# Kernel tuning notes

Measured on AMD Instinct MI355X. Metric: run time of the kernel, lower is better.

## Reference

```python
import jax, jax.numpy as jnp
import numpy as np
import math

HIDDEN = 1024
EXPAND = 2
INNER = HIDDEN * EXPAND          # 2048
STATE = 16
K = 4                            # conv kernel size
DT_RANK = math.ceil(HIDDEN / 16) # 64
DT_MIN, DT_MAX = 1e-3, 0.1


def setup_inputs() -> dict:
    key = jax.random.key(0)
    ks = jax.random.split(key, 10)
    B, L = 2, 1024
    hidden_states = jax.random.normal(ks[0], (B, L, HIDDEN), dtype=jnp.float32)
    # parameters (torch Linear weight stored transposed -> we use [in, out])
    W_in = jax.random.normal(ks[1], (HIDDEN, 2 * INNER), dtype=jnp.float32) * (HIDDEN ** -0.5)
    conv_w = jax.random.normal(ks[2], (K, INNER), dtype=jnp.float32) * (K ** -0.5)   # depthwise
    conv_b = jax.random.normal(ks[3], (INNER,), dtype=jnp.float32) * 0.02
    W_xproj = jax.random.normal(ks[4], (INNER, DT_RANK + 2 * STATE), dtype=jnp.float32) * (INNER ** -0.5)
    dt_init_std = DT_RANK ** -0.5
    W_dt = jax.random.uniform(ks[5], (DT_RANK, INNER), dtype=jnp.float32,
                              minval=-dt_init_std, maxval=dt_init_std)
    dt = jnp.exp(jax.random.uniform(ks[6], (INNER,), dtype=jnp.float32)
                 * (math.log(DT_MAX) - math.log(DT_MIN)) + math.log(DT_MIN))
    dt = jnp.clip(dt, 1e-4, None)
    b_dt = dt + jnp.log(-jnp.expm1(-dt))   # inverse softplus init
    A = jnp.tile(jnp.arange(1, STATE + 1, dtype=jnp.float32)[None, :], (INNER, 1))
    A_log = jnp.log(A)
    D = jnp.ones((INNER,), dtype=jnp.float32)
    W_out = jax.random.normal(ks[7], (INNER, HIDDEN), dtype=jnp.float32) * (INNER ** -0.5)
    return {"hidden_states": hidden_states, "W_in": W_in, "conv_w": conv_w,
            "conv_b": conv_b, "W_xproj": W_xproj, "W_dt": W_dt, "b_dt": b_dt,
            "A_log": A_log, "D": D, "W_out": W_out}


def _silu(x):
    return x * jax.nn.sigmoid(x)


def _mamba_forward(hidden_states, W_in, conv_w, conv_b, W_xproj, W_dt, b_dt, A_log, D, W_out):
    Bsz, L, _ = hidden_states.shape
    xz = hidden_states @ W_in                # [B, L, 2*inner]
    x, z = jnp.split(xz, 2, axis=-1)         # each [B, L, inner]

    # causal depthwise conv along L (torch Conv1d pad=K-1, truncated to seq_len)
    xp = jnp.pad(x, ((0, 0), (K - 1, 0), (0, 0)))
    xc = conv_b
    for k in range(K):                       # K=4 fixed, unrolled
        xc = xc + xp[:, k:k + L, :] * conv_w[k]
    x = _silu(xc)                            # [B, L, inner]

    # selective SSM
    A = -jnp.exp(A_log)                      # [inner, state]
    xproj = x @ W_xproj                      # [B, L, dt_rank + 2*state]
    dt, Bm, Cm = jnp.split(xproj, [DT_RANK, DT_RANK + STATE], axis=-1)
    dt = jax.nn.softplus(dt @ W_dt + b_dt)   # [B, L, inner]

    deltaA = jnp.exp(dt[..., None] * A)                                   # [B, L, inner, state]
    deltaBx = dt[..., None] * Bm[:, :, None, :] * x[..., None]            # [B, L, inner, state]

    def step(h, inp):
        dA, dBx, c = inp                     # [B,inner,state],[B,inner,state],[B,state]
        h = dA * h + dBx
        y = jnp.einsum('bdn,bn->bd', h, c)   # [B, inner]
        return h, y

    h0 = jnp.zeros((Bsz, INNER, STATE), dtype=x.dtype)
    _, ys = jax.lax.scan(step, h0, (jnp.moveaxis(deltaA, 1, 0),
                                    jnp.moveaxis(deltaBx, 1, 0),
                                    jnp.moveaxis(Cm, 1, 0)))
    y = jnp.moveaxis(ys, 0, 1)               # [B, L, inner]
    y = y + x * D
    y = y * _silu(z)
    return y @ W_out                         # [B, L, hidden]


def reference(hidden_states, W_in, conv_w, conv_b, W_xproj, W_dt, b_dt, A_log, D, W_out):
    return _mamba_forward(hidden_states, W_in, conv_w, conv_b, W_xproj, W_dt, b_dt, A_log, D, W_out)
```

## Files before the change

### kernel.cpp

```cpp
#include <hip/hip_runtime.h>
#include <math.h>

#define HID    1024
#define INNER  2048
#define NROWS  2048
#define LSEQ   1024
#define STATE  16
#define DTR    64
#define XPN    96
#define NC     32
#define LC     32
#define KSPLIT 16
#define KCH    128

typedef __attribute__((ext_vector_type(8))) short bf16x8;
typedef __attribute__((ext_vector_type(4))) float f32x4;

#define GLDS16(g, l) __builtin_amdgcn_global_load_lds( \
    (const __attribute__((address_space(1))) unsigned int*)(g), \
    (__attribute__((address_space(3))) unsigned int*)(l), 16, 0, 0)

__device__ __forceinline__ float siluf(float x) { return x / (1.f + __expf(-x)); }

__device__ __forceinline__ short f2bf(float f) {
    unsigned u = __float_as_uint(f);
    unsigned r = (u + 0x7FFFu + ((u >> 16) & 1u)) >> 16;
    return (short)r;
}
__device__ __forceinline__ float bf2f(short s) {
    return __uint_as_float(((unsigned)(unsigned short)s) << 16);
}

template<int N> __device__ __forceinline__ void wait_vm() {
    if      constexpr (N == 0) asm volatile("s_waitcnt vmcnt(0)" ::: "memory");
    else if constexpr (N == 2) asm volatile("s_waitcnt vmcnt(2)" ::: "memory");
    else if constexpr (N == 3) asm volatile("s_waitcnt vmcnt(3)" ::: "memory");
    else if constexpr (N == 4) asm volatile("s_waitcnt vmcnt(4)" ::: "memory");
}

__global__ __launch_bounds__(256) void prep1(
    const float* __restrict__ hs, short* __restrict__ hs16,
    const float* __restrict__ W_in, short* __restrict__ W_inT,
    const float* __restrict__ W_xp, short* __restrict__ W_xpT,
    const float* __restrict__ W_dt, short* __restrict__ W_dtT,
    const float* __restrict__ W_out, short* __restrict__ W_outT)
{
    int blk = blockIdx.x;
    if (blk < 2048) {
        int i = blk * 256 + threadIdx.x;
        float4 v = ((const float4*)hs)[i];
        union { short s[4]; int2 p; } o;
        o.s[0] = f2bf(v.x); o.s[1] = f2bf(v.y); o.s[2] = f2bf(v.z); o.s[3] = f2bf(v.w);
        ((int2*)hs16)[i] = o.p;
        return;
    }
    blk -= 2048;
    const float* W; short* Wt; int K, N, bx, by;
    if (blk < 4096)        { W = W_in;  Wt = W_inT;  K = 1024; N = 4096; bx = blk & 127; by = blk >> 7; }
    else if (blk < 4288)   { int t = blk - 4096; W = W_xp;  Wt = W_xpT;  K = 2048; N = 96;   bx = t % 3;  by = t / 3; }
    else if (blk < 4416)   { int t = blk - 4288; W = W_dt;  Wt = W_dtT;  K = 64;   N = 2048; bx = t & 63; by = t >> 6; }
    else                   { int t = blk - 4416; W = W_out; Wt = W_outT; K = 2048; N = 1024; bx = t & 31; by = t >> 5; }
    __shared__ float tile[32][33];
    int bn = bx * 32, bk = by * 32;
    int tx = threadIdx.x & 31, ty = threadIdx.x >> 5;
#pragma unroll
    for (int i = 0; i < 32; i += 8)
        tile[ty + i][tx] = W[(size_t)(bk + ty + i) * N + bn + tx];
    __syncthreads();
#pragma unroll
    for (int i = 0; i < 32; i += 8)
        Wt[(size_t)(bn + ty + i) * K + bk + tx] = f2bf(tile[tx][ty + i]);
}

template<int BM, int BN, int EPI>
__global__ __launch_bounds__(256) void gemm_p(
    const short* __restrict__ A, const short* __restrict__ Bt,
    void* __restrict__ Cout, int M, int N, int K,
    const float* __restrict__ bias)
{
    constexpr int NI = BM / 32;
    constexpr int NJ = BN / 32;
    constexpr int LPB = BM / 64 + BN / 64;
    __shared__ short As[3][BM * 32];
    __shared__ short Bs[3][BN * 32];
    const int tid = threadIdx.x;
    const int lane = tid & 63;
    const int wv = tid >> 6;
    const int wm = (wv >> 1) * (BM / 2), wn = (wv & 1) * (BN / 2);
    const int bm = blockIdx.y * BM, bn = blockIdx.x * BN;
    const int l16 = lane & 15, lhi = lane >> 4;
    const size_t arow0 = (size_t)(bm + wv * 16 + (lane >> 2)) * K + (lane & 3) * 8;
    const size_t brow0 = (size_t)(bn + wv * 16 + (lane >> 2)) * K + (lane & 3) * 8;

    auto stage = [&](int buf, int koff) {
        GLDS16(&A[arow0 + koff], &As[buf][(wv * 16) * 32]);
        if (BM == 128) GLDS16(&A[arow0 + (size_t)64 * K + koff], &As[buf][(64 + wv * 16) * 32]);
        GLDS16(&Bt[brow0 + koff], &Bs[buf][(wv * 16) * 32]);
        if (BN == 128) GLDS16(&Bt[brow0 + (size_t)64 * K + koff], &Bs[buf][(64 + wv * 16) * 32]);
    };

    f32x4 acc[NI][NJ] = {};
    const int nt = K / 32;
    stage(0, 0);
    if (nt > 1) stage(1, 32);
    for (int t = 0; t < nt; ++t) {
        if (t == nt - 1) wait_vm<0>();
        else             wait_vm<LPB>();
        __builtin_amdgcn_s_barrier();
        __builtin_amdgcn_sched_barrier(0);
        if (t + 2 < nt) stage((t + 2) % 3, (t + 2) * 32);
        const int cur = t % 3;
        bf16x8 af[NI], bfr[NJ];
#pragma unroll
        for (int i = 0; i < NI; ++i)
            af[i] = *(const bf16x8*)&As[cur][(wm + i * 16 + l16) * 32 + lhi * 8];
#pragma unroll
        for (int j = 0; j < NJ; ++j)
            bfr[j] = *(const bf16x8*)&Bs[cur][(wn + j * 16 + l16) * 32 + lhi * 8];
#pragma unroll
        for (int i = 0; i < NI; ++i)
#pragma unroll
            for (int j = 0; j < NJ; ++j)
                acc[i][j] = __builtin_amdgcn_mfma_f32_16x16x32_bf16(af[i], bfr[j], acc[i][j], 0, 0, 0);
    }
#pragma unroll
    for (int i = 0; i < NI; ++i)
#pragma unroll
        for (int j = 0; j < NJ; ++j)
#pragma unroll
            for (int r = 0; r < 4; ++r) {
                int row = bm + wm + i * 16 + lhi * 4 + r;
                int col = bn + wn + j * 16 + l16;
                float v = acc[i][j][r];
                if (EPI == 0) {
                    ((float*)Cout)[(size_t)row * N + col] = v;
                } else if (EPI == 1) {
                    v += bias[col];
                    v = (v > 20.f) ? v : log1pf(__expf(v));
                    ((short*)Cout)[(size_t)row * N + col] = f2bf(v);
                } else {
                    ((short*)Cout)[(size_t)row * N + col] = f2bf(v);
                }
            }
}

__global__ __launch_bounds__(256) void gemm_xproj(
    const short* __restrict__ A, const short* __restrict__ Bt,
    float* __restrict__ partial)
{
    __shared__ short As[4][64][40];
    __shared__ short Bs[4][96][40];
    const int tid = threadIdx.x;
    const int lane = tid & 63;
    const int wv = tid >> 6;
    const int l16 = lane & 15, lhi = lane >> 4;
    const int bm = blockIdx.x * 64;
    const int kc = blockIdx.y;
    const int k0 = kc * KCH;
    const int r = tid >> 2, cs = (tid & 3) * 8;
#pragma unroll
    for (int ks = 0; ks < 4; ++ks)
        *(int4*)&As[ks][r][cs] = *(const int4*)&A[(size_t)(bm + r) * INNER + k0 + ks * 32 + cs];
#pragma unroll
    for (int ks = 0; ks < 4; ++ks)
        *(int4*)&Bs[ks][r][cs] = *(const int4*)&Bt[(size_t)r * INNER + k0 + ks * 32 + cs];
    if (tid < 128) {
        int r2 = 64 + (tid >> 2);
#pragma unroll
        for (int ks = 0; ks < 4; ++ks)
            *(int4*)&Bs[ks][r2][cs] = *(const int4*)&Bt[(size_t)r2 * INNER + k0 + ks * 32 + cs];
    }
    __syncthreads();
    f32x4 acc[6] = {};
#pragma unroll
    for (int ks = 0; ks < 4; ++ks) {
        bf16x8 a = *(const bf16x8*)&As[ks][wv * 16 + l16][lhi * 8];
#pragma unroll
        for (int j = 0; j < 6; ++j) {
            bf16x8 b = *(const bf16x8*)&Bs[ks][j * 16 + l16][lhi * 8];
            acc[j] = __builtin_amdgcn_mfma_f32_16x16x32_bf16(a, b, acc[j], 0, 0, 0);
        }
    }
    size_t base = (size_t)kc * ((size_t)NROWS * XPN);
#pragma unroll
    for (int j = 0; j < 6; ++j)
#pragma unroll
        for (int rr = 0; rr < 4; ++rr) {
            int row = bm + wv * 16 + lhi * 4 + rr;
            int col = j * 16 + l16;
            partial[base + (size_t)row * XPN + col] = acc[j][rr];
        }
}

__global__ __launch_bounds__(256) void xproj_reduce(
    const float* __restrict__ partial, float* __restrict__ xproj,
    short* __restrict__ xprojb)
{
    int idx = blockIdx.x * 256 + threadIdx.x;
    if (idx >= NROWS * XPN) return;
    float s = 0.f;
#pragma unroll
    for (int kc = 0; kc < KSPLIT; ++kc)
        s += partial[(size_t)kc * ((size_t)NROWS * XPN) + idx];
    xproj[idx] = s;
    int row = idx / XPN;
    int col = idx - row * XPN;
    if (col < DTR) xprojb[row * DTR + col] = f2bf(s);
}

__global__ __launch_bounds__(256) void conv_silu(
    const short* __restrict__ xzb,
    const float* __restrict__ conv_w,
    const float* __restrict__ conv_b,
    short* __restrict__ xconvb)
{
    int idx = blockIdx.x * 256 + threadIdx.x;
    int d4 = (idx & 511) << 2;
    int row = idx >> 9;
    int l = row & (LSEQ - 1);
    int rowbase = row - l;
    float4 acc = *(const float4*)&conv_b[d4];
#pragma unroll
    for (int k = 0; k < 4; ++k) {
        int ls = l - 3 + k;
        if (ls >= 0) {
            union { short s[4]; int2 p; } xi;
            xi.p = *(const int2*)&xzb[(size_t)(rowbase + ls) * (2 * INNER) + d4];
            float4 w = *(const float4*)&conv_w[k * INNER + d4];
            acc.x = fmaf(bf2f(xi.s[0]), w.x, acc.x);
            acc.y = fmaf(bf2f(xi.s[1]), w.y, acc.y);
            acc.z = fmaf(bf2f(xi.s[2]), w.z, acc.z);
            acc.w = fmaf(bf2f(xi.s[3]), w.w, acc.w);
        }
    }
    union { short s[4]; int2 p; } o;
    o.s[0] = f2bf(siluf(acc.x)); o.s[1] = f2bf(siluf(acc.y));
    o.s[2] = f2bf(siluf(acc.z)); o.s[3] = f2bf(siluf(acc.w));
    *(int2*)&xconvb[(size_t)row * INNER + d4] = o.p;
}

__global__ __launch_bounds__(256) void scan_phaseA(
    const short* __restrict__ dtb, const float* __restrict__ xproj,
    const short* __restrict__ xconvb, const float* __restrict__ A_log,
    float* __restrict__ hend, float* __restrict__ sdA)
{
    int idx = blockIdx.x * 256 + threadIdx.x;
    int d = idx & (INNER - 1);
    int c = (idx >> 11) & (NC - 1);
    int b = idx >> 16;
    float A_dn[STATE];
    {
        const float4* Ap = (const float4*)&A_log[d * STATE];
        float4 a0 = Ap[0], a1 = Ap[1], a2 = Ap[2], a3 = Ap[3];
        float al[16] = {a0.x,a0.y,a0.z,a0.w, a1.x,a1.y,a1.z,a1.w,
                        a2.x,a2.y,a2.z,a2.w, a3.x,a3.y,a3.z,a3.w};
#pragma unroll
        for (int n = 0; n < STATE; ++n) A_dn[n] = -__expf(al[n]);
    }
    float h[STATE] = {};
    float sdt = 0.f;
    int row0 = b * LSEQ + c * LC;
    for (int l = 0; l < LC; ++l) {
        size_t row = row0 + l;
        float dtv = bf2f(dtb[row * INNER + d]);
        float xv  = bf2f(xconvb[row * INNER + d]);
        const float4* Bp = (const float4*)&xproj[row * XPN + DTR];
        float4 b0 = Bp[0], b1 = Bp[1], b2 = Bp[2], b3 = Bp[3];
        float Bv[16] = {b0.x,b0.y,b0.z,b0.w, b1.x,b1.y,b1.z,b1.w,
                        b2.x,b2.y,b2.z,b2.w, b3.x,b3.y,b3.z,b3.w};
        float dtx = dtv * xv;
        sdt += dtv;
#pragma unroll
        for (int n = 0; n < STATE; ++n)
            h[n] = fmaf(__expf(dtv * A_dn[n]), h[n], dtx * Bv[n]);
    }
    size_t o = ((size_t)(b * NC + c) * INNER + d) * STATE;
#pragma unroll
    for (int n = 0; n < STATE; ++n) hend[o + n] = h[n];
#pragma unroll
    for (int n = 0; n < STATE; ++n) sdA[o + n] = A_dn[n] * sdt;
}

__global__ __launch_bounds__(256) void scan_phaseB(
    float* __restrict__ hend, const float* __restrict__ sdA)
{
    int idx = blockIdx.x * 256 + threadIdx.x;
    int b = idx >> 15;
    int dn = idx & 32767;
    float H = 0.f;
#pragma unroll
    for (int c = 0; c < NC; ++c) {
        size_t o = (size_t)(b * NC + c) * (INNER * STATE) + dn;
        float m = hend[o];
        hend[o] = H;
        H = fmaf(__expf(sdA[o]), H, m);
    }
}

__global__ __launch_bounds__(256) void scan_phaseC(
    const short* __restrict__ dtb, const float* __restrict__ xproj,
    const short* __restrict__ xconvb, const short* __restrict__ xzb,
    const float* __restrict__ A_log, const float* __restrict__ Dp,
    const float* __restrict__ Hinit, short* __restrict__ yactb)
{
    int idx = blockIdx.x * 256 + threadIdx.x;
    int d = idx & (INNER - 1);
    int c = (idx >> 11) & (NC - 1);
    int b = idx >> 16;
    float A_dn[STATE];
    {
        const float4* Ap = (const float4*)&A_log[d * STATE];
        float4 a0 = Ap[0], a1 = Ap[1], a2 = Ap[2], a3 = Ap[3];
        float al[16] = {a0.x,a0.y,a0.z,a0.w, a1.x,a1.y,a1.z,a1.w,
                        a2.x,a2.y,a2.z,a2.w, a3.x,a3.y,a3.z,a3.w};
#pragma unroll
        for (int n = 0; n < STATE; ++n) A_dn[n] = -__expf(al[n]);
    }
    float Dd = Dp[d];
    float h[STATE];
    {
        const float4* Hp = (const float4*)&Hinit[((size_t)(b * NC + c) * INNER + d) * STATE];
        float4 h0 = Hp[0], h1 = Hp[1], h2 = Hp[2], h3 = Hp[3];
        h[0]=h0.x; h[1]=h0.y; h[2]=h0.z; h[3]=h0.w;
        h[4]=h1.x; h[5]=h1.y; h[6]=h1.z; h[7]=h1.w;
        h[8]=h2.x; h[9]=h2.y; h[10]=h2.z; h[11]=h2.w;
        h[12]=h3.x; h[13]=h3.y; h[14]=h3.z; h[15]=h3.w;
    }
    int row0 = b * LSEQ + c * LC;
    for (int l = 0; l < LC; ++l) {
        size_t row = row0 + l;
        float dtv = bf2f(dtb[row * INNER + d]);
        float xv  = bf2f(xconvb[row * INNER + d]);
        float zv  = bf2f(xzb[row * (2 * INNER) + INNER + d]);
        const float4* Bp = (const float4*)&xproj[row * XPN + DTR];
        float4 b0 = Bp[0], b1 = Bp[1], b2 = Bp[2], b3 = Bp[3];
        float4 c0 = Bp[4], c1 = Bp[5], c2 = Bp[6], c3 = Bp[7];
        float Bv[16] = {b0.x,b0.y,b0.z,b0.w, b1.x,b1.y,b1.z,b1.w,
                        b2.x,b2.y,b2.z,b2.w, b3.x,b3.y,b3.z,b3.w};
        float Cv[16] = {c0.x,c0.y,c0.z,c0.w, c1.x,c1.y,c1.z,c1.w,
                        c2.x,c2.y,c2.z,c2.w, c3.x,c3.y,c3.z,c3.w};
        float dtx = dtv * xv;
        float s0 = 0.f, s1 = 0.f;
#pragma unroll
        for (int n = 0; n < STATE; ++n) {
            h[n] = fmaf(__expf(dtv * A_dn[n]), h[n], dtx * Bv[n]);
            if (n & 1) s1 = fmaf(h[n], Cv[n], s1);
            else       s0 = fmaf(h[n], Cv[n], s0);
        }
        float y = s0 + s1 + xv * Dd;
        yactb[row * INNER + d] = f2bf(y * siluf(zv));
    }
}

extern "C" void kernel_launch(void* const* d_in, const int* in_sizes, int n_in,
                              void* d_out, int out_size, void* d_ws, size_t ws_size,
                              hipStream_t stream) {
    const float* hs     = (const float*)d_in[0];
    const float* W_in   = (const float*)d_in[1];
    const float* conv_w = (const float*)d_in[2];
    const float* conv_b = (const float*)d_in[3];
    const float* W_xp   = (const float*)d_in[4];
    const float* W_dt   = (const float*)d_in[5];
    const float* b_dt   = (const float*)d_in[6];
    const float* A_log  = (const float*)d_in[7];
    const float* Dp     = (const float*)d_in[8];
    const float* W_out  = (const float*)d_in[9];
    float* out = (float*)d_out;

    float* xproj   = (float*)d_ws;
    float* hend    = xproj + (size_t)NROWS * XPN;
    float* sdA     = hend  + (size_t)2 * NC * INNER * STATE;
    float* partial = sdA   + (size_t)2 * NC * INNER * STATE;
    short* hs16    = (short*)(partial + (size_t)KSPLIT * NROWS * XPN);
    short* xzb     = hs16   + (size_t)NROWS * HID;
    short* xconvb  = xzb    + (size_t)NROWS * 2 * INNER;
    short* dtb     = xconvb + (size_t)NROWS * INNER;
    short* yactb   = dtb    + (size_t)NROWS * INNER;
    short* WinT    = yactb  + (size_t)NROWS * INNER;
    short* WoutT   = WinT   + (size_t)4096 * HID;
    short* WxpT    = WoutT  + (size_t)HID * INNER;
    short* WdtT    = WxpT   + (size_t)XPN * INNER;
    short* xprojb  = WdtT   + (size_t)INNER * DTR;

    dim3 blk(256);

    prep1<<<2048 + 4096 + 192 + 128 + 2048, blk, 0, stream>>>(
        hs, hs16, W_in, WinT, W_xp, WxpT, W_dt, WdtT, W_out, WoutT);
    gemm_p<128, 128, 2><<<dim3(4096 / 128, NROWS / 128), blk, 0, stream>>>(
        hs16, WinT, xzb, NROWS, 2 * INNER, HID, nullptr);
    conv_silu<<<(NROWS * INNER / 4) / 256, blk, 0, stream>>>(xzb, conv_w, conv_b, xconvb);
    gemm_xproj<<<dim3(NROWS / 64, KSPLIT), blk, 0, stream>>>(xconvb, WxpT, partial);
    xproj_reduce<<<(NROWS * XPN) / 256, blk, 0, stream>>>(partial, xproj, xprojb);
    gemm_p<128, 64, 1><<<dim3(INNER / 64, NROWS / 128), blk, 0, stream>>>(
        xprojb, WdtT, dtb, NROWS, INNER, DTR, b_dt);
    scan_phaseA<<<(2 * NC * INNER) / 256, blk, 0, stream>>>(
        dtb, xproj, xconvb, A_log, hend, sdA);
    scan_phaseB<<<(2 * INNER * STATE) / 256, blk, 0, stream>>>(hend, sdA);
    scan_phaseC<<<(2 * NC * INNER) / 256, blk, 0, stream>>>(
        dtb, xproj, xconvb, xzb, A_log, Dp, hend, yactb);
    gemm_p<64, 64, 0><<<dim3(HID / 64, NROWS / 64), blk, 0, stream>>>(
        yactb, WoutT, out, NROWS, HID, INNER, nullptr);
}
```

Measured before the change: 164.7 us.

## Shrink scan carry traffic, widen conv vectors, halve xproj split, swizzle GEMM blocks

Scan phase A now stores one summed dt per (batch, chunk, channel) instead of a full per-state sdA tensor. Phase B recomputes A from A_log and forms the decay exponent itself, which removes a large write and read of intermediate state. The conv+silu kernel handles 8 channels per thread with 16-byte loads. The x-projection split-K is halved so each block loops over two 128-wide K chunks, and the generic GEMM gains a block-index swizzle for cache locality. The costs are extra exp work in phase B, fewer blocks in gemm_xproj, and scalar conv_w loads.

```diff
diff --git a/kernel.cpp b/kernel.cpp
--- a/kernel.cpp
+++ b/kernel.cpp
@@ -10,8 +10,8 @@
 #define XPN    96
 #define NC     32
 #define LC     32
-#define KSPLIT 16
-#define KCH    128
+#define KSPLIT 8
+#define KCH    256
 
 typedef __attribute__((ext_vector_type(8))) short bf16x8;
 typedef __attribute__((ext_vector_type(4))) float f32x4;
@@ -83,11 +83,15 @@
     constexpr int LPB = BM / 64 + BN / 64;
     __shared__ short As[3][BM * 32];
     __shared__ short Bs[3][BN * 32];
+    const int gx = gridDim.x;
+    const int nwg = gx * gridDim.y;
+    const int bid = blockIdx.y * gx + blockIdx.x;
+    const int swz = (bid & 7) * (nwg >> 3) + (bid >> 3);
+    const int bm = (swz / gx) * BM, bn = (swz % gx) * BN;
     const int tid = threadIdx.x;
     const int lane = tid & 63;
     const int wv = tid >> 6;
     const int wm = (wv >> 1) * (BM / 2), wn = (wv & 1) * (BN / 2);
-    const int bm = blockIdx.y * BM, bn = blockIdx.x * BN;
     const int l16 = lane & 15, lhi = lane >> 4;
     const size_t arow0 = (size_t)(bm + wv * 16 + (lane >> 2)) * K + (lane & 3) * 8;
     const size_t brow0 = (size_t)(bn + wv * 16 + (lane >> 2)) * K + (lane & 3) * 8;
@@ -156,29 +160,33 @@
     const int l16 = lane & 15, lhi = lane >> 4;
     const int bm = blockIdx.x * 64;
     const int kc = blockIdx.y;
-    const int k0 = kc * KCH;
     const int r = tid >> 2, cs = (tid & 3) * 8;
-#pragma unroll
-    for (int ks = 0; ks < 4; ++ks)
-        *(int4*)&As[ks][r][cs] = *(const int4*)&A[(size_t)(bm + r) * INNER + k0 + ks * 32 + cs];
-#pragma unroll
-    for (int ks = 0; ks < 4; ++ks)
-        *(int4*)&Bs[ks][r][cs] = *(const int4*)&Bt[(size_t)r * INNER + k0 + ks * 32 + cs];
-    if (tid < 128) {
-        int r2 = 64 + (tid >> 2);
+    f32x4 acc[6] = {};
+#pragma unroll
+    for (int half = 0; half < 2; ++half) {
+        const int k0 = kc * KCH + half * 128;
+        if (half) __syncthreads();
 #pragma unroll
         for (int ks = 0; ks < 4; ++ks)
-            *(int4*)&Bs[ks][r2][cs] = *(const int4*)&Bt[(size_t)r2 * INNER + k0 + ks * 32 + cs];
-    }
-    __syncthreads();
-    f32x4 acc[6] = {};
-#pragma unroll
-    for (int ks = 0; ks < 4; ++ks) {
-        bf16x8 a = *(const bf16x8*)&As[ks][wv * 16 + l16][lhi * 8];
-#pragma unroll
-        for (int j = 0; j < 6; ++j) {
-            bf16x8 b = *(const bf16x8*)&Bs[ks][j * 16 + l16][lhi * 8];
-            acc[j] = __builtin_amdgcn_mfma_f32_16x16x32_bf16(a, b, acc[j], 0, 0, 0);
+            *(int4*)&As[ks][r][cs] = *(const int4*)&A[(size_t)(bm + r) * INNER + k0 + ks * 32 + cs];
+#pragma unroll
+        for (int ks = 0; ks < 4; ++ks)
+            *(int4*)&Bs[ks][r][cs] = *(const int4*)&Bt[(size_t)r * INNER + k0 + ks * 32 + cs];
+        if (tid < 128) {
+            int r2 = 64 + (tid >> 2);
+#pragma unroll
+            for (int ks = 0; ks < 4; ++ks)
+                *(int4*)&Bs[ks][r2][cs] = *(const int4*)&Bt[(size_t)r2 * INNER + k0 + ks * 32 + cs];
+        }
+        __syncthreads();
+#pragma unroll
+        for (int ks = 0; ks < 4; ++ks) {
+            bf16x8 a = *(const bf16x8*)&As[ks][wv * 16 + l16][lhi * 8];
+#pragma unroll
+            for (int j = 0; j < 6; ++j) {
+                bf16x8 b = *(const bf16x8*)&Bs[ks][j * 16 + l16][lhi * 8];
+                acc[j] = __builtin_amdgcn_mfma_f32_16x16x32_bf16(a, b, acc[j], 0, 0, 0);
+            }
         }
     }
     size_t base = (size_t)kc * ((size_t)NROWS * XPN);
@@ -215,34 +223,34 @@
     short* __restrict__ xconvb)
 {
     int idx = blockIdx.x * 256 + threadIdx.x;
-    int d4 = (idx & 511) << 2;
-    int row = idx >> 9;
+    int d8 = (idx & 255) << 3;
+    int row = idx >> 8;
     int l = row & (LSEQ - 1);
     int rowbase = row - l;
-    float4 acc = *(const float4*)&conv_b[d4];
+    float acc[8];
+#pragma unroll
+    for (int j = 0; j < 8; ++j) acc[j] = conv_b[d8 + j];
 #pragma unroll
     for (int k = 0; k < 4; ++k) {
         int ls = l - 3 + k;
         if (ls >= 0) {
-            union { short s[4]; int2 p; } xi;
-            xi.p = *(const int2*)&xzb[(size_t)(rowbase + ls) * (2 * INNER) + d4];
-            float4 w = *(const float4*)&conv_w[k * INNER + d4];
-            acc.x = fmaf(bf2f(xi.s[0]), w.x, acc.x);
-            acc.y = fmaf(bf2f(xi.s[1]), w.y, acc.y);
-            acc.z = fmaf(bf2f(xi.s[2]), w.z, acc.z);
-            acc.w = fmaf(bf2f(xi.s[3]), w.w, acc.w);
+            union { short s[8]; int4 p; } xi;
+            xi.p = *(const int4*)&xzb[(size_t)(rowbase + ls) * (2 * INNER) + d8];
+#pragma unroll
+            for (int j = 0; j < 8; ++j)
+                acc[j] = fmaf(bf2f(xi.s[j]), conv_w[k * INNER + d8 + j], acc[j]);
         }
     }
-    union { short s[4]; int2 p; } o;
-    o.s[0] = f2bf(siluf(acc.x)); o.s[1] = f2bf(siluf(acc.y));
-    o.s[2] = f2bf(siluf(acc.z)); o.s[3] = f2bf(siluf(acc.w));
-    *(int2*)&xconvb[(size_t)row * INNER + d4] = o.p;
+    union { short s[8]; int4 p; } o;
+#pragma unroll
+    for (int j = 0; j < 8; ++j) o.s[j] = f2bf(siluf(acc[j]));
+    *(int4*)&xconvb[(size_t)row * INNER + d8] = o.p;
 }
 
 __global__ __launch_bounds__(256) void scan_phaseA(
     const short* __restrict__ dtb, const float* __restrict__ xproj,
     const short* __restrict__ xconvb, const float* __restrict__ A_log,
-    float* __restrict__ hend, float* __restrict__ sdA)
+    float* __restrict__ hend, float* __restrict__ sdt_out)
 {
     int idx = blockIdx.x * 256 + threadIdx.x;
     int d = idx & (INNER - 1);
@@ -277,23 +285,26 @@
     size_t o = ((size_t)(b * NC + c) * INNER + d) * STATE;
 #pragma unroll
     for (int n = 0; n < STATE; ++n) hend[o + n] = h[n];
-#pragma unroll
-    for (int n = 0; n < STATE; ++n) sdA[o + n] = A_dn[n] * sdt;
+    sdt_out[(size_t)(b * NC + c) * INNER + d] = sdt;
 }
 
 __global__ __launch_bounds__(256) void scan_phaseB(
-    float* __restrict__ hend, const float* __restrict__ sdA)
+    float* __restrict__ hend, const float* __restrict__ sdt,
+    const float* __restrict__ A_log)
 {
     int idx = blockIdx.x * 256 + threadIdx.x;
     int b = idx >> 15;
     int dn = idx & 32767;
+    int d = dn >> 4, n = dn & 15;
+    float A_dn = -__expf(A_log[d * STATE + n]);
     float H = 0.f;
 #pragma unroll
     for (int c = 0; c < NC; ++c) {
         size_t o = (size_t)(b * NC + c) * (INNER * STATE) + dn;
         float m = hend[o];
         hend[o] = H;
-        H = fmaf(__expf(sdA[o]), H, m);
+        float s = sdt[(size_t)(b * NC + c) * INNER + d];
+        H = fmaf(__expf(s * A_dn), H, m);
     }
 }
 
@@ -369,8 +380,8 @@
 
     float* xproj   = (float*)d_ws;
     float* hend    = xproj + (size_t)NROWS * XPN;
-    float* sdA     = hend  + (size_t)2 * NC * INNER * STATE;
-    float* partial = sdA   + (size_t)2 * NC * INNER * STATE;
+    float* sdt     = hend  + (size_t)2 * NC * INNER * STATE;
+    float* partial = sdt   + (size_t)2 * NC * INNER;
     short* hs16    = (short*)(partial + (size_t)KSPLIT * NROWS * XPN);
     short* xzb     = hs16   + (size_t)NROWS * HID;
     short* xconvb  = xzb    + (size_t)NROWS * 2 * INNER;
@@ -388,14 +399,14 @@
         hs, hs16, W_in, WinT, W_xp, WxpT, W_dt, WdtT, W_out, WoutT);
     gemm_p<128, 128, 2><<<dim3(4096 / 128, NROWS / 128), blk, 0, stream>>>(
         hs16, WinT, xzb, NROWS, 2 * INNER, HID, nullptr);
-    conv_silu<<<(NROWS * INNER / 4) / 256, blk, 0, stream>>>(xzb, conv_w, conv_b, xconvb);
+    conv_silu<<<(NROWS * INNER / 8) / 256, blk, 0, stream>>>(xzb, conv_w, conv_b, xconvb);
     gemm_xproj<<<dim3(NROWS / 64, KSPLIT), blk, 0, stream>>>(xconvb, WxpT, partial);
     xproj_reduce<<<(NROWS * XPN) / 256, blk, 0, stream>>>(partial, xproj, xprojb);
     gemm_p<128, 64, 1><<<dim3(INNER / 64, NROWS / 128), blk, 0, stream>>>(
         xprojb, WdtT, dtb, NROWS, INNER, DTR, b_dt);
     scan_phaseA<<<(2 * NC * INNER) / 256, blk, 0, stream>>>(
-        dtb, xproj, xconvb, A_log, hend, sdA);
-    scan_phaseB<<<(2 * INNER * STATE) / 256, blk, 0, stream>>>(hend, sdA);
+        dtb, xproj, xconvb, A_log, hend, sdt);
+    scan_phaseB<<<(2 * INNER * STATE) / 256, blk, 0, stream>>>(hend, sdt, A_log);
     scan_phaseC<<<(2 * NC * INNER) / 256, blk, 0, stream>>>(
         dtb, xproj, xconvb, xzb, A_log, Dp, hend, yactb);
     gemm_p<64, 64, 0><<<dim3(HID / 64, NROWS / 64), blk, 0, stream>>>(
```

New measurement: 162.8 us. Within noise of the previous version (-1.2%).
